# Optimization experiments

Hardware: AMD Instinct MI355X
Metric: run time of the kernel (lower is better)

## Reference

```python
import jax, jax.numpy as jnp
import numpy as np

D_MODEL = 1024
H = 16
DK = D_MODEL // H
D_FC = 4096
B = 2
S = 1024
EPS = 1e-6


def setup_inputs() -> dict:
    key = jax.random.key(0)
    ks = jax.random.split(key, 8)
    sc = 1.0 / np.sqrt(D_MODEL)
    return {
        "x": jax.random.normal(ks[0], (B, S, D_MODEL), dtype=jnp.float32),
        "mask": jnp.ones((B, 1, 1, S), dtype=jnp.int32),
        "w_q": jax.random.normal(ks[1], (D_MODEL, D_MODEL), dtype=jnp.float32) * sc,
        "w_k": jax.random.normal(ks[2], (D_MODEL, D_MODEL), dtype=jnp.float32) * sc,
        "w_v": jax.random.normal(ks[3], (D_MODEL, D_MODEL), dtype=jnp.float32) * sc,
        "w_o": jax.random.normal(ks[4], (D_MODEL, D_MODEL), dtype=jnp.float32) * sc,
        "alpha1": jnp.ones((D_MODEL,), dtype=jnp.float32),
        "beta1": jnp.zeros((D_MODEL,), dtype=jnp.float32),
        "alpha2": jnp.ones((D_MODEL,), dtype=jnp.float32),
        "beta2": jnp.zeros((D_MODEL,), dtype=jnp.float32),
        "fc1_w": jax.random.normal(ks[5], (D_FC, D_MODEL), dtype=jnp.float32) * sc,
        "fc1_b": jnp.zeros((D_FC,), dtype=jnp.float32),
        "fc2_w": jax.random.normal(ks[6], (D_MODEL, D_FC), dtype=jnp.float32) * (1.0 / np.sqrt(D_FC)),
        "fc2_b": jnp.zeros((D_MODEL,), dtype=jnp.float32),
    }


def _layernorm(x, alpha, beta):
    # Matches torch: mean and std (unbiased, ddof=1), divide by (std + eps)
    mean = jnp.mean(x, axis=-1, keepdims=True)
    std = jnp.std(x, axis=-1, keepdims=True, ddof=1)
    return alpha * (x - mean) / (std + EPS) + beta


def _mha(x, mask, w_q, w_k, w_v, w_o):
    # nn.Linear(bias=False): y = x @ W.T
    q = (x @ w_q.T).reshape(B, S, H, DK).transpose(0, 2, 1, 3)  # (B,H,S,DK)
    k = (x @ w_k.T).reshape(B, S, H, DK).transpose(0, 2, 1, 3)
    v = (x @ w_v.T).reshape(B, S, H, DK).transpose(0, 2, 1, 3)
    scores = jnp.einsum('bhqd,bhkd->bhqk', q, k) / jnp.sqrt(jnp.float32(DK))
    scores = jnp.where(mask == 0, jnp.float32(-1e9), scores)
    attn = jax.nn.softmax(scores, axis=-1)  # dropout=0 (eval)
    out = jnp.einsum('bhqk,bhkd->bhqd', attn, v)  # (B,H,S,DK)
    out = out.transpose(0, 2, 1, 3).reshape(B, S, D_MODEL)
    return out @ w_o.T


def _ffn(x, fc1_w, fc1_b, fc2_w, fc2_b):
    h = jax.nn.relu(x @ fc1_w.T + fc1_b)
    return h @ fc2_w.T + fc2_b


def reference(x, mask, w_q, w_k, w_v, w_o, alpha1, beta1, alpha2, beta2,
              fc1_w, fc1_b, fc2_w, fc2_b):
    # Pre-LN residual block 1: attention
    x = x + _mha(_layernorm(x, alpha1, beta1), mask, w_q, w_k, w_v, w_o)
    # Pre-LN residual block 2: FFN
    x = x + _ffn(_layernorm(x, alpha2, beta2), fc1_w, fc1_b, fc2_w, fc2_b)
    return x
```

## Files before the change

kernel.cpp:

```cpp
#include <hip/hip_runtime.h>
#include <hip/hip_bf16.h>


typedef __bf16 bf16;
typedef __attribute__((ext_vector_type(8))) __bf16 bf16x8;
typedef __attribute__((ext_vector_type(4))) __bf16 bf16x4;
typedef __attribute__((ext_vector_type(4))) float f32x4;

#define NTOK 2048
#define DM   1024
#define DFC  4096
#define QKVN 3072

__device__ inline void gl_lds16(const void* g, void* l) {
    __builtin_amdgcn_global_load_lds((const __attribute__((address_space(1))) void*)g,
                                     (__attribute__((address_space(3))) void*)l, 16, 0, 0);
}

__global__ __launch_bounds__(256) void f2b_all_kernel(
    const float4* __restrict__ wq, const float4* __restrict__ wk,
    const float4* __restrict__ wv, const float4* __restrict__ wo,
    const float4* __restrict__ f1, const float4* __restrict__ f2,
    bf16x4* __restrict__ oqkv, bf16x4* __restrict__ oo,
    bf16x4* __restrict__ of1, bf16x4* __restrict__ of2) {
    int i = blockIdx.x * 256 + threadIdx.x;
    const int Q = 262144;
    float4 v;
    bf16x4* dst;
    if (i < 3 * Q) {
        v = (i < Q) ? wq[i] : (i < 2 * Q) ? wk[i - Q] : wv[i - 2 * Q];
        dst = oqkv + i;
    } else if (i < 4 * Q) {
        v = wo[i - 3 * Q];
        dst = oo + (i - 3 * Q);
    } else if (i < 8 * Q) {
        v = f1[i - 4 * Q];
        dst = of1 + (i - 4 * Q);
    } else {
        v = f2[i - 8 * Q];
        dst = of2 + (i - 8 * Q);
    }
    bf16x4 o;
    o[0] = (bf16)v.x; o[1] = (bf16)v.y; o[2] = (bf16)v.z; o[3] = (bf16)v.w;
    *dst = o;
}

__device__ inline void ln_row(float4 v, const float* alpha, const float* beta,
                              bf16* outrow, int t) {
    float s  = v.x + v.y + v.z + v.w;
    float ss = v.x * v.x + v.y * v.y + v.z * v.z + v.w * v.w;
    __shared__ float red[8];
    int lane = t & 63, wv = t >> 6;
    #pragma unroll
    for (int o = 32; o > 0; o >>= 1) {
        s  += __shfl_down(s, o);
        ss += __shfl_down(ss, o);
    }
    if (lane == 0) { red[wv] = s; red[4 + wv] = ss; }
    __syncthreads();
    float S  = red[0] + red[1] + red[2] + red[3];
    float SS = red[4] + red[5] + red[6] + red[7];
    float mean = S * (1.0f / 1024.0f);
    float var  = (SS - S * mean) * (1.0f / 1023.0f);
    var = var < 0.f ? 0.f : var;
    float inv = 1.0f / (sqrtf(var) + 1e-6f);
    float4 a4 = reinterpret_cast<const float4*>(alpha)[t];
    float4 b4 = reinterpret_cast<const float4*>(beta)[t];
    bf16x4 o4;
    o4[0] = (bf16)(a4.x * (v.x - mean) * inv + b4.x);
    o4[1] = (bf16)(a4.y * (v.y - mean) * inv + b4.y);
    o4[2] = (bf16)(a4.z * (v.z - mean) * inv + b4.z);
    o4[3] = (bf16)(a4.w * (v.w - mean) * inv + b4.w);
    reinterpret_cast<bf16x4*>(outrow)[t] = o4;
}

__global__ __launch_bounds__(256) void ln_kernel(const float* __restrict__ x,
                                                 const float* __restrict__ alpha,
                                                 const float* __restrict__ beta,
                                                 bf16* __restrict__ out) {
    int row = blockIdx.x, t = threadIdx.x;
    float4 v = reinterpret_cast<const float4*>(x + (size_t)row * DM)[t];
    ln_row(v, alpha, beta, out + (size_t)row * DM, t);
}

__global__ __launch_bounds__(256) void reduce_ln_kernel(const float* __restrict__ p,
                                                        const float* __restrict__ resid,
                                                        const float* __restrict__ alpha,
                                                        const float* __restrict__ beta,
                                                        float* __restrict__ x2,
                                                        bf16* __restrict__ xn) {
    int row = blockIdx.x, t = threadIdx.x;
    size_t i4 = (size_t)row * 256 + t;
    float4 a = reinterpret_cast<const float4*>(p)[i4];
    float4 b = reinterpret_cast<const float4*>(p)[i4 + 524288];
    float4 r = reinterpret_cast<const float4*>(resid)[i4];
    float4 v;
    v.x = a.x + b.x + r.x; v.y = a.y + b.y + r.y;
    v.z = a.z + b.z + r.z; v.w = a.w + b.w + r.w;
    reinterpret_cast<float4*>(x2)[i4] = v;
    ln_row(v, alpha, beta, xn + (size_t)row * DM, t);
}

__global__ __launch_bounds__(256) void reduce_out_kernel(const float* __restrict__ p,
                                                         const float* __restrict__ bias,
                                                         const float* __restrict__ x2,
                                                         float* __restrict__ out) {
    size_t i4 = (size_t)blockIdx.x * 256 + threadIdx.x;
    float4 a = reinterpret_cast<const float4*>(p)[i4];
    float4 b = reinterpret_cast<const float4*>(p)[i4 + 524288];
    float4 r = reinterpret_cast<const float4*>(x2)[i4];
    float4 bi = reinterpret_cast<const float4*>(bias)[i4 & 255];
    float4 o;
    o.x = a.x + b.x + r.x + bi.x; o.y = a.y + b.y + r.y + bi.y;
    o.z = a.z + b.z + r.z + bi.z; o.w = a.w + b.w + r.w + bi.w;
    reinterpret_cast<float4*>(out)[i4] = o;
}

template <int EPI>
__global__ __launch_bounds__(256) void gemm128(const bf16* __restrict__ A,
                                               const bf16* __restrict__ Bt,
                                               void* __restrict__ outp,
                                               const float* __restrict__ bias,
                                               int M, int N, int K, int kslice) {
    __shared__ bf16 As[128 * 64];
    __shared__ bf16 Bs[128 * 64];
    int tid = threadIdx.x;
    int lane = tid & 63, wave = tid >> 6;
    int q = lane >> 4, r = lane & 15;
    int wm = wave >> 1, wn = wave & 1;
    int m0 = blockIdx.y * 128, n0 = blockIdx.x * 128;
    int kbeg = blockIdx.z * kslice, kend = kbeg + kslice;
    f32x4 acc[4][4] = {};

    int srow = tid >> 3;
    int csrc = (tid & 7) ^ (srow & 7);
    const bf16* agp = A  + (size_t)(m0 + srow) * K + csrc * 8;
    const bf16* bgp = Bt + (size_t)(n0 + srow) * K + csrc * 8;
    bf16* alp = As + tid * 8;
    bf16* blp = Bs + tid * 8;

    int rsw = (r & 7);
    int co0 = ((q ^ rsw) * 8);
    int co1 = co0 ^ 32;
    const bf16* ara = As + (wm * 64 + r) * 64;
    const bf16* brb = Bs + (wn * 64 + r) * 64;

    for (int k0 = kbeg; k0 < kend; k0 += 64) {
        #pragma unroll
        for (int j = 0; j < 4; ++j) {
            gl_lds16(agp + (size_t)j * 32 * K + k0, alp + j * 2048);
            gl_lds16(bgp + (size_t)j * 32 * K + k0, blp + j * 2048);
        }
        __syncthreads();
        #pragma unroll
        for (int half = 0; half < 2; ++half) {
            int co = half ? co1 : co0;
            bf16x8 af[4], bfv[4];
            #pragma unroll
            for (int t = 0; t < 4; ++t)
                af[t] = *reinterpret_cast<const bf16x8*>(ara + t * 1024 + co);
            #pragma unroll
            for (int u = 0; u < 4; ++u)
                bfv[u] = *reinterpret_cast<const bf16x8*>(brb + u * 1024 + co);
            #pragma unroll
            for (int t = 0; t < 4; ++t)
                #pragma unroll
                for (int u = 0; u < 4; ++u)
                    acc[t][u] = __builtin_amdgcn_mfma_f32_16x16x32_bf16(af[t], bfv[u], acc[t][u], 0, 0, 0);
        }
        __syncthreads();
    }

    size_t zoff = (size_t)blockIdx.z * M * N;
    #pragma unroll
    for (int t = 0; t < 4; ++t) {
        #pragma unroll
        for (int u = 0; u < 4; ++u) {
            #pragma unroll
            for (int i = 0; i < 4; ++i) {
                int mm = m0 + wm * 64 + t * 16 + q * 4 + i;
                int nn = n0 + wn * 64 + u * 16 + r;
                size_t idx = (size_t)mm * N + nn;
                float v = acc[t][u][i];
                if (EPI == 0) {
                    ((bf16*)outp)[idx] = (bf16)v;
                } else if (EPI == 1) {
                    v += bias[nn];
                    ((bf16*)outp)[idx] = (bf16)(v > 0.f ? v : 0.f);
                } else {
                    ((float*)outp)[zoff + idx] = v;
                }
            }
        }
    }
}

__global__ void transpose_v(const bf16* __restrict__ qkv, bf16* __restrict__ vt) {
    __shared__ bf16 tile[32][33];
    int bh = blockIdx.z;
    int b = bh >> 4, h = bh & 15;
    int s0 = blockIdx.x * 32;
    int d0 = blockIdx.y * 32;
    int tx = threadIdx.x, ty = threadIdx.y;
    tile[ty][tx] = qkv[(size_t)(b * 1024 + s0 + ty) * QKVN + 2048 + h * 64 + d0 + tx];
    __syncthreads();
    vt[(size_t)(bh * 64 + d0 + ty) * 1024 + s0 + tx] = tile[tx][ty];
}

__global__ __launch_bounds__(256) void attn_kernel(const bf16* __restrict__ qkv,
                                                   const bf16* __restrict__ Vt,
                                                   const int* __restrict__ mask,
                                                   bf16* __restrict__ out) {
    __shared__ bf16 Ks[2][4096];
    __shared__ bf16 Vs[2][4096];
    __shared__ bf16 pbuf[4][1024];
    __shared__ float msk[1024];
    int tid = threadIdx.x;
    int lane = tid & 63, w = tid >> 6;
    int q = lane >> 4, r = lane & 15;
    int id = blockIdx.x;
    int qb = id & 15, h = (id >> 4) & 15, b = id >> 8;

    {
        int4 mi = reinterpret_cast<const int4*>(mask + b * 1024)[tid];
        msk[tid * 4 + 0] = mi.x ? 0.f : -1e9f;
        msk[tid * 4 + 1] = mi.y ? 0.f : -1e9f;
        msk[tid * 4 + 2] = mi.z ? 0.f : -1e9f;
        msk[tid * 4 + 3] = mi.w ? 0.f : -1e9f;
    }

    const bf16* qrow = qkv + (size_t)(b * 1024 + qb * 64 + w * 16 + r) * QKVN + h * 64 + q * 8;
    bf16x8 qf0 = *reinterpret_cast<const bf16x8*>(qrow);
    bf16x8 qf1 = *reinterpret_cast<const bf16x8*>(qrow + 32);

    int csw = (tid & 7) ^ ((tid >> 3) & 7);
    const bf16* kg0 = qkv + (size_t)(b * 1024 + (tid >> 3)) * QKVN + 1024 + h * 64 + csw * 8;
    const bf16* kg1 = kg0 + (size_t)32 * QKVN;
    const bf16* vg0 = Vt + (size_t)((b * 16 + h) * 64 + (tid >> 3)) * 1024 + csw * 8;
    const bf16* vg1 = vg0 + 32 * 1024;
    bf16* kld = &Ks[0][tid * 8];
    bf16* vld = &Vs[0][tid * 8];

    int co0 = (q ^ (r & 7)) * 8;
    bf16* pw = pbuf[w];

    float m[4] = {-1e30f, -1e30f, -1e30f, -1e30f};
    float l[4] = {0.f, 0.f, 0.f, 0.f};
    f32x4 o[4] = {};

    gl_lds16(kg0, kld);
    gl_lds16(kg1, kld + 2048);
    gl_lds16(vg0, vld);
    gl_lds16(vg1, vld + 2048);

    for (int t = 0; t < 16; ++t) {
        __syncthreads();
        if (t < 15) {
            int ktn = (t + 1) * 64;
            int bo = ((t + 1) & 1) * 4096;
            gl_lds16(kg0 + (size_t)ktn * QKVN, kld + bo);
            gl_lds16(kg1 + (size_t)ktn * QKVN, kld + bo + 2048);
            gl_lds16(vg0 + ktn, vld + bo);
            gl_lds16(vg1 + ktn, vld + bo + 2048);
        }
        const bf16* Kb = Ks[t & 1];
        const bf16* Vb = Vs[t & 1];
        int kt = t * 64;

        f32x4 s[4];
        #pragma unroll
        for (int ks = 0; ks < 4; ++ks) {
            bf16x8 kf0 = *reinterpret_cast<const bf16x8*>(&Kb[(ks * 16 + r) * 64 + co0]);
            bf16x8 kf1 = *reinterpret_cast<const bf16x8*>(&Kb[(ks * 16 + r) * 64 + (co0 ^ 32)]);
            f32x4 a = {};
            a = __builtin_amdgcn_mfma_f32_16x16x32_bf16(qf0, kf0, a, 0, 0, 0);
            a = __builtin_amdgcn_mfma_f32_16x16x32_bf16(qf1, kf1, a, 0, 0, 0);
            float mb = msk[kt + ks * 16 + r];
            #pragma unroll
            for (int i = 0; i < 4; ++i) s[ks][i] = fmaf(a[i], 0.125f, mb);
        }
        float alpha[4];
        #pragma unroll
        for (int i = 0; i < 4; ++i) {
            float t2 = fmaxf(fmaxf(s[0][i], s[1][i]), fmaxf(s[2][i], s[3][i]));
            t2 = fmaxf(t2, __shfl_xor(t2, 1));
            t2 = fmaxf(t2, __shfl_xor(t2, 2));
            t2 = fmaxf(t2, __shfl_xor(t2, 4));
            t2 = fmaxf(t2, __shfl_xor(t2, 8));
            float mn = fmaxf(m[i], t2);
            alpha[i] = __expf(m[i] - mn);
            m[i] = mn;
        }
        #pragma unroll
        for (int i = 0; i < 4; ++i) {
            float e0 = __expf(s[0][i] - m[i]);
            float e1 = __expf(s[1][i] - m[i]);
            float e2 = __expf(s[2][i] - m[i]);
            float e3 = __expf(s[3][i] - m[i]);
            s[0][i] = e0; s[1][i] = e1; s[2][i] = e2; s[3][i] = e3;
            float rs = (e0 + e1) + (e2 + e3);
            rs += __shfl_xor(rs, 1);
            rs += __shfl_xor(rs, 2);
            rs += __shfl_xor(rs, 4);
            rs += __shfl_xor(rs, 8);
            l[i] = l[i] * alpha[i] + rs;
        }
        #pragma unroll
        for (int nt = 0; nt < 4; ++nt)
            #pragma unroll
            for (int i = 0; i < 4; ++i) o[nt][i] *= alpha[i];
        #pragma unroll
        for (int ks = 0; ks < 4; ++ks) {
            int kc = ks * 2 + (r >> 3);
            #pragma unroll
            for (int i = 0; i < 4; ++i) {
                int mr = q * 4 + i;
                pw[mr * 64 + ((kc ^ (mr & 7)) * 8) + (r & 7)] = (bf16)s[ks][i];
            }
        }
        #pragma unroll
        for (int ks2 = 0; ks2 < 2; ++ks2) {
            int vpo = (((ks2 * 4 + q) ^ (r & 7)) * 8);
            bf16x8 pf = *reinterpret_cast<const bf16x8*>(&pw[r * 64 + vpo]);
            #pragma unroll
            for (int nt = 0; nt < 4; ++nt) {
                bf16x8 vf = *reinterpret_cast<const bf16x8*>(&Vb[(nt * 16 + r) * 64 + vpo]);
                o[nt] = __builtin_amdgcn_mfma_f32_16x16x32_bf16(pf, vf, o[nt], 0, 0, 0);
            }
        }
    }

    float inv[4];
    #pragma unroll
    for (int i = 0; i < 4; ++i) inv[i] = 1.0f / l[i];
    #pragma unroll
    for (int nt = 0; nt < 4; ++nt)
        #pragma unroll
        for (int i = 0; i < 4; ++i)
            out[(size_t)(b * 1024 + qb * 64 + w * 16 + q * 4 + i) * DM + h * 64 + nt * 16 + r] =
                (bf16)(o[nt][i] * inv[i]);
}

extern "C" void kernel_launch(void* const* d_in, const int* in_sizes, int n_in,
                              void* d_out, int out_size, void* d_ws, size_t ws_size,
                              hipStream_t stream) {
    const float* x      = (const float*)d_in[0];
    const int*   mask   = (const int*)  d_in[1];
    const float* w_q    = (const float*)d_in[2];
    const float* w_k    = (const float*)d_in[3];
    const float* w_v    = (const float*)d_in[4];
    const float* w_o    = (const float*)d_in[5];
    const float* alpha1 = (const float*)d_in[6];
    const float* beta1  = (const float*)d_in[7];
    const float* alpha2 = (const float*)d_in[8];
    const float* beta2  = (const float*)d_in[9];
    const float* fc1_w  = (const float*)d_in[10];
    const float* fc1_b  = (const float*)d_in[11];
    const float* fc2_w  = (const float*)d_in[12];
    const float* fc2_b  = (const float*)d_in[13];
    float* out = (float*)d_out;

    char* ws = (char*)d_ws;
    const size_t MB = 1024 * 1024;
    bf16*  wqkv_b = (bf16*)(ws +  0 * MB);
    bf16*  wo_b   = (bf16*)(ws +  6 * MB);
    bf16*  f1w_b  = (bf16*)(ws +  8 * MB);
    bf16*  f2w_b  = (bf16*)(ws + 16 * MB);
    bf16*  xn     = (bf16*)(ws + 24 * MB);
    bf16*  qkvb   = (bf16*)(ws + 28 * MB);
    bf16*  vtb    = (bf16*)(ws + 40 * MB);
    bf16*  attnb  = (bf16*)(ws + 44 * MB);
    float* x2     = (float*)(ws + 48 * MB);
    float* po     = (float*)(ws + 28 * MB);
    bf16*  hb     = (bf16*)(ws + 28 * MB);
    float* pf2    = (float*)(ws +  0 * MB);

    f2b_all_kernel<<<12288, 256, 0, stream>>>(
        (const float4*)w_q, (const float4*)w_k, (const float4*)w_v, (const float4*)w_o,
        (const float4*)fc1_w, (const float4*)fc2_w,
        (bf16x4*)wqkv_b, (bf16x4*)wo_b, (bf16x4*)f1w_b, (bf16x4*)f2w_b);

    ln_kernel<<<NTOK, 256, 0, stream>>>(x, alpha1, beta1, xn);

    gemm128<0><<<dim3(QKVN / 128, NTOK / 128, 1), 256, 0, stream>>>(
        xn, wqkv_b, qkvb, nullptr, NTOK, QKVN, DM, DM);

    transpose_v<<<dim3(32, 2, 32), dim3(32, 32), 0, stream>>>(qkvb, vtb);

    attn_kernel<<<512, 256, 0, stream>>>(qkvb, vtb, mask, attnb);

    gemm128<4><<<dim3(DM / 128, NTOK / 128, 2), 256, 0, stream>>>(
        attnb, wo_b, po, nullptr, NTOK, DM, DM, DM / 2);

    reduce_ln_kernel<<<NTOK, 256, 0, stream>>>(po, x, alpha2, beta2, x2, xn);

    gemm128<1><<<dim3(DFC / 128, NTOK / 128, 1), 256, 0, stream>>>(
        xn, f1w_b, hb, fc1_b, NTOK, DFC, DM, DM);

    gemm128<4><<<dim3(DM / 128, NTOK / 128, 2), 256, 0, stream>>>(
        hb, f2w_b, pf2, nullptr, NTOK, DM, DFC, DFC / 2);

    reduce_out_kernel<<<2048, 256, 0, stream>>>(pf2, fc2_b, x2, out);
}
```

Measured before the change: 274.3 us.

## Double-buffer GEMM LDS tiles and fuse weight conversion with first layernorm

The GEMM now uses two LDS buffers and issues the global-to-LDS loads for the next K tile before computing on the current one. This drops one barrier per iteration and overlaps memory latency with MFMA work, at the cost of twice the shared memory per block, which can lower occupancy. Separately, the weight fp32-to-bf16 conversion and the first layernorm are merged into one launch to remove a kernel launch gap.

After: 262.7 us. 4.2% less time.

```diff
diff --git a/kernel.cpp b/kernel.cpp
--- a/kernel.cpp
+++ b/kernel.cpp
@@ -15,34 +15,6 @@
 __device__ inline void gl_lds16(const void* g, void* l) {
     __builtin_amdgcn_global_load_lds((const __attribute__((address_space(1))) void*)g,
                                      (__attribute__((address_space(3))) void*)l, 16, 0, 0);
-}
-
-__global__ __launch_bounds__(256) void f2b_all_kernel(
-    const float4* __restrict__ wq, const float4* __restrict__ wk,
-    const float4* __restrict__ wv, const float4* __restrict__ wo,
-    const float4* __restrict__ f1, const float4* __restrict__ f2,
-    bf16x4* __restrict__ oqkv, bf16x4* __restrict__ oo,
-    bf16x4* __restrict__ of1, bf16x4* __restrict__ of2) {
-    int i = blockIdx.x * 256 + threadIdx.x;
-    const int Q = 262144;
-    float4 v;
-    bf16x4* dst;
-    if (i < 3 * Q) {
-        v = (i < Q) ? wq[i] : (i < 2 * Q) ? wk[i - Q] : wv[i - 2 * Q];
-        dst = oqkv + i;
-    } else if (i < 4 * Q) {
-        v = wo[i - 3 * Q];
-        dst = oo + (i - 3 * Q);
-    } else if (i < 8 * Q) {
-        v = f1[i - 4 * Q];
-        dst = of1 + (i - 4 * Q);
-    } else {
-        v = f2[i - 8 * Q];
-        dst = of2 + (i - 8 * Q);
-    }
-    bf16x4 o;
-    o[0] = (bf16)v.x; o[1] = (bf16)v.y; o[2] = (bf16)v.z; o[3] = (bf16)v.w;
-    *dst = o;
 }
 
 __device__ inline void ln_row(float4 v, const float* alpha, const float* beta,
@@ -74,13 +46,42 @@
     reinterpret_cast<bf16x4*>(outrow)[t] = o4;
 }
 
-__global__ __launch_bounds__(256) void ln_kernel(const float* __restrict__ x,
-                                                 const float* __restrict__ alpha,
-                                                 const float* __restrict__ beta,
-                                                 bf16* __restrict__ out) {
-    int row = blockIdx.x, t = threadIdx.x;
-    float4 v = reinterpret_cast<const float4*>(x + (size_t)row * DM)[t];
-    ln_row(v, alpha, beta, out + (size_t)row * DM, t);
+__global__ __launch_bounds__(256) void prep_kernel(
+    const float4* __restrict__ wq, const float4* __restrict__ wk,
+    const float4* __restrict__ wv, const float4* __restrict__ wo,
+    const float4* __restrict__ f1, const float4* __restrict__ f2,
+    bf16x4* __restrict__ oqkv, bf16x4* __restrict__ oo,
+    bf16x4* __restrict__ of1, bf16x4* __restrict__ of2,
+    const float* __restrict__ x, const float* __restrict__ alpha1,
+    const float* __restrict__ beta1, bf16* __restrict__ xn) {
+    int blk = blockIdx.x;
+    int t = threadIdx.x;
+    if (blk < 12288) {
+        int i = blk * 256 + t;
+        const int Q = 262144;
+        float4 v;
+        bf16x4* dst;
+        if (i < 3 * Q) {
+            v = (i < Q) ? wq[i] : (i < 2 * Q) ? wk[i - Q] : wv[i - 2 * Q];
+            dst = oqkv + i;
+        } else if (i < 4 * Q) {
+            v = wo[i - 3 * Q];
+            dst = oo + (i - 3 * Q);
+        } else if (i < 8 * Q) {
+            v = f1[i - 4 * Q];
+            dst = of1 + (i - 4 * Q);
+        } else {
+            v = f2[i - 8 * Q];
+            dst = of2 + (i - 8 * Q);
+        }
+        bf16x4 o;
+        o[0] = (bf16)v.x; o[1] = (bf16)v.y; o[2] = (bf16)v.z; o[3] = (bf16)v.w;
+        *dst = o;
+    } else {
+        int row = blk - 12288;
+        float4 v = reinterpret_cast<const float4*>(x + (size_t)row * DM)[t];
+        ln_row(v, alpha1, beta1, xn + (size_t)row * DM, t);
+    }
 }
 
 __global__ __launch_bounds__(256) void reduce_ln_kernel(const float* __restrict__ p,
@@ -122,53 +123,59 @@
                                                void* __restrict__ outp,
                                                const float* __restrict__ bias,
                                                int M, int N, int K, int kslice) {
-    __shared__ bf16 As[128 * 64];
-    __shared__ bf16 Bs[128 * 64];
+    __shared__ bf16 As[2][128 * 64];
+    __shared__ bf16 Bs[2][128 * 64];
     int tid = threadIdx.x;
     int lane = tid & 63, wave = tid >> 6;
     int q = lane >> 4, r = lane & 15;
     int wm = wave >> 1, wn = wave & 1;
     int m0 = blockIdx.y * 128, n0 = blockIdx.x * 128;
-    int kbeg = blockIdx.z * kslice, kend = kbeg + kslice;
+    int kbeg = blockIdx.z * kslice;
+    int nit = kslice / 64;
     f32x4 acc[4][4] = {};
 
     int srow = tid >> 3;
     int csrc = (tid & 7) ^ (srow & 7);
-    const bf16* agp = A  + (size_t)(m0 + srow) * K + csrc * 8;
-    const bf16* bgp = Bt + (size_t)(n0 + srow) * K + csrc * 8;
-    bf16* alp = As + tid * 8;
-    bf16* blp = Bs + tid * 8;
+    const bf16* agp = A  + (size_t)(m0 + srow) * K + kbeg + csrc * 8;
+    const bf16* bgp = Bt + (size_t)(n0 + srow) * K + kbeg + csrc * 8;
 
     int rsw = (r & 7);
     int co0 = ((q ^ rsw) * 8);
     int co1 = co0 ^ 32;
-    const bf16* ara = As + (wm * 64 + r) * 64;
-    const bf16* brb = Bs + (wn * 64 + r) * 64;
-
-    for (int k0 = kbeg; k0 < kend; k0 += 64) {
+    int aoff = (wm * 64 + r) * 64;
+    int boff = (wn * 64 + r) * 64;
+
+    auto stage = [&](int it, int b) {
+        int k0 = it * 64;
         #pragma unroll
         for (int j = 0; j < 4; ++j) {
-            gl_lds16(agp + (size_t)j * 32 * K + k0, alp + j * 2048);
-            gl_lds16(bgp + (size_t)j * 32 * K + k0, blp + j * 2048);
-        }
+            gl_lds16(agp + (size_t)j * 32 * K + k0, &As[b][tid * 8 + j * 2048]);
+            gl_lds16(bgp + (size_t)j * 32 * K + k0, &Bs[b][tid * 8 + j * 2048]);
+        }
+    };
+
+    stage(0, 0);
+    for (int it = 0; it < nit; ++it) {
         __syncthreads();
+        if (it + 1 < nit) stage(it + 1, (it + 1) & 1);
+        const bf16* Ab = &As[it & 1][aoff];
+        const bf16* Bb = &Bs[it & 1][boff];
         #pragma unroll
         for (int half = 0; half < 2; ++half) {
             int co = half ? co1 : co0;
             bf16x8 af[4], bfv[4];
             #pragma unroll
             for (int t = 0; t < 4; ++t)
-                af[t] = *reinterpret_cast<const bf16x8*>(ara + t * 1024 + co);
+                af[t] = *reinterpret_cast<const bf16x8*>(Ab + t * 1024 + co);
             #pragma unroll
             for (int u = 0; u < 4; ++u)
-                bfv[u] = *reinterpret_cast<const bf16x8*>(brb + u * 1024 + co);
+                bfv[u] = *reinterpret_cast<const bf16x8*>(Bb + u * 1024 + co);
             #pragma unroll
             for (int t = 0; t < 4; ++t)
                 #pragma unroll
                 for (int u = 0; u < 4; ++u)
                     acc[t][u] = __builtin_amdgcn_mfma_f32_16x16x32_bf16(af[t], bfv[u], acc[t][u], 0, 0, 0);
         }
-        __syncthreads();
     }
 
     size_t zoff = (size_t)blockIdx.z * M * N;
@@ -375,12 +382,11 @@
     bf16*  hb     = (bf16*)(ws + 28 * MB);
     float* pf2    = (float*)(ws +  0 * MB);
 
-    f2b_all_kernel<<<12288, 256, 0, stream>>>(
+    prep_kernel<<<14336, 256, 0, stream>>>(
         (const float4*)w_q, (const float4*)w_k, (const float4*)w_v, (const float4*)w_o,
         (const float4*)fc1_w, (const float4*)fc2_w,
-        (bf16x4*)wqkv_b, (bf16x4*)wo_b, (bf16x4*)f1w_b, (bf16x4*)f2w_b);
-
-    ln_kernel<<<NTOK, 256, 0, stream>>>(x, alpha1, beta1, xn);
+        (bf16x4*)wqkv_b, (bf16x4*)wo_b, (bf16x4*)f1w_b, (bf16x4*)f2w_b,
+        x, alpha1, beta1, xn);
 
     gemm128<0><<<dim3(QKVN / 128, NTOK / 128, 1), 256, 0, stream>>>(
         xn, wqkv_b, qkvb, nullptr, NTOK, QKVN, DM, DM);
```
